# Performance work log

Measured on AMD Instinct MI355X. Metric: run time of the kernel, lower is better.

The kernel has to match this reference:

```python
import jax, jax.numpy as jnp
import numpy as np

T, B, NHID = 64, 32, 768
NB, BS = 6, 128          # num_blocks, block_size = nhid // num_blocks
TOPK = 4                 # active blocks per step
NTOK = 32000
ATT = 4 * BS             # input-attention value dim (att_out), per RIMs BlocksCore
DK = 64                  # input-attention key dim
NH2, DK2 = 4, 16         # communication attention heads / head dim


def setup_inputs() -> dict:
    key = jax.random.key(0)
    ks = jax.random.split(key, 16)
    s = 0.02
    return {
        "x": jax.random.normal(ks[0], (T, B, NHID), jnp.float32),
        "hx0": jax.random.normal(ks[1], (B, NHID), jnp.float32),
        "cx0": jax.random.normal(ks[2], (B, NHID), jnp.float32),
        # input attention (1 head): per-read-block query proj, per-write-slot key/value proj
        "Wq_in": jax.random.normal(ks[3], (NB, BS, DK), jnp.float32) * s,
        "Wk_in": jax.random.normal(ks[4], (2, NHID, DK), jnp.float32) * s,
        "Wv_in": jax.random.normal(ks[5], (2, NHID, ATT), jnp.float32) * s,
        # block-diagonal LSTM (blockify_params): per-block weights
        "Wih": jax.random.normal(ks[6], (NB, ATT, 4 * BS), jnp.float32) * s,
        "Whh": jax.random.normal(ks[7], (NB, BS, 4 * BS), jnp.float32) * s,
        "b_lstm": jnp.zeros((NB, 4 * BS), jnp.float32),
        # communication attention (4 heads, dk=dv=16), per-block projections + output proj
        "Wq_c": jax.random.normal(ks[8], (NB, BS, NH2 * DK2), jnp.float32) * s,
        "Wk_c": jax.random.normal(ks[9], (NB, BS, NH2 * DK2), jnp.float32) * s,
        "Wv_c": jax.random.normal(ks[10], (NB, BS, NH2 * DK2), jnp.float32) * s,
        "Wo_c": jax.random.normal(ks[11], (NB, NH2 * DK2, BS), jnp.float32) * s,
        # decoder
        "Wd": jax.random.normal(ks[12], (NTOK, NHID), jnp.float32) * 0.1,
        "bd": jnp.zeros((NTOK,), jnp.float32),
    }


def _step(hx, cx, xt, Wq_in, Wk_in, Wv_in, Wih, Whh, b_lstm, Wq_c, Wk_c, Wv_c, Wo_c):
    hb = hx.reshape(B, NB, BS)
    cb = cx.reshape(B, NB, BS)
    # --- input attention: each block reads from {null, input} slots ---
    kv_in = jnp.stack([jnp.zeros_like(xt), xt], axis=1)          # [B,2,NHID]
    q = jnp.einsum('bnd,ndk->bnk', hb, Wq_in)                    # [B,NB,DK]
    k = jnp.einsum('bmd,mdk->bmk', kv_in, Wk_in)                 # [B,2,DK]
    v = jnp.einsum('bmd,mdv->bmv', kv_in, Wv_in)                 # [B,2,ATT]
    iatt = jax.nn.softmax(
        jnp.einsum('bnk,bmk->bnm', q, k) / jnp.sqrt(jnp.float32(DK)), axis=-1)
    inp_use = jnp.einsum('bnm,bmv->bnv', iatt, v)                # [B,NB,ATT]
    # --- top-k block routing: drop NB-TOPK blocks attending most to null ---
    null_att = iatt[:, :, 0]                                     # [B,NB]
    _, drop_idx = jax.lax.top_k(null_att, NB - TOPK)
    mask = jnp.ones((B, NB), hx.dtype).at[
        jnp.arange(B)[:, None], drop_idx].set(0.0)               # [B,NB]
    # --- per-block (block-diagonal) LSTM ---
    gates = (jnp.einsum('bnv,nvg->bng', inp_use, Wih)
             + jnp.einsum('bnh,nhg->bng', hb, Whh) + b_lstm)     # [B,NB,4*BS]
    i, f, g, o = jnp.split(gates, 4, axis=-1)
    c_new = jax.nn.sigmoid(f) * cb + jax.nn.sigmoid(i) * jnp.tanh(g)
    h_new = jax.nn.sigmoid(o) * jnp.tanh(c_new)                  # [B,NB,BS]
    # --- communication attention among blocks (residual) ---
    q2 = jnp.einsum('bnd,ndk->bnk', h_new, Wq_c).reshape(B, NB, NH2, DK2)
    k2 = jnp.einsum('bnd,ndk->bnk', h_new, Wk_c).reshape(B, NB, NH2, DK2)
    v2 = jnp.einsum('bnd,ndk->bnk', h_new, Wv_c).reshape(B, NB, NH2, DK2)
    att = jax.nn.softmax(
        jnp.einsum('bihk,bjhk->bhij', q2, k2) / jnp.sqrt(jnp.float32(DK2)), axis=-1)
    comm = jnp.einsum('bhij,bjhv->bihv', att, v2).reshape(B, NB, NH2 * DK2)
    h_new = h_new + jnp.einsum('bnk,nkd->bnd', comm, Wo_c)
    # --- gated state update: inactive blocks keep old state ---
    m = mask[:, :, None]
    hx_next = (m * h_new + (1.0 - m) * hb).reshape(B, NHID)
    cx_next = (m * c_new + (1.0 - m) * cb).reshape(B, NHID)
    return hx_next, cx_next


def reference(x, hx0, cx0, Wq_in, Wk_in, Wv_in, Wih, Whh, b_lstm,
              Wq_c, Wk_c, Wv_c, Wo_c, Wd, bd):
    def scan_step(carry, xt):
        hx, cx = carry
        hx, cx = _step(hx, cx, xt, Wq_in, Wk_in, Wv_in, Wih, Whh, b_lstm,
                       Wq_c, Wk_c, Wv_c, Wo_c)
        return (hx, cx), hx
    (hx, cx), outs = jax.lax.scan(scan_step, (hx0, cx0), x)     # outs: [T,B,NHID]
    decoded = outs.reshape(T * B, NHID) @ Wd.T + bd              # [T*B,NTOK]
    return decoded, hx, cx
```

## Files before the change

kernel.cpp:

```cpp
#include <hip/hip_runtime.h>
#include <hip/hip_bf16.h>
#include <stdint.h>

#define TT 64
#define BB 32
#define NHIDC 768
#define NBK 6
#define BSZ 128
#define NTOKC 32000

using f32x4  = __attribute__((ext_vector_type(4))) float;
using f32x2  = __attribute__((ext_vector_type(2))) float;
using short8 = __attribute__((ext_vector_type(8))) short;
typedef unsigned long long u64;

#define OFF_XPUB  4096u
#define OFF_WTH   1048576u
#define OFF_WTL   4194304u
#define OFF_HTB   8065024u
#define OFF_K1    11210752u
#define OFF_V1H   11735040u
#define OFF_V1L   13832192u
#define OFF_U     15929344u
#define OFF_WDB   41095168u

__device__ __forceinline__ float sigf(float x){ return 1.f/(1.f + expf(-x)); }

__device__ __forceinline__ void stp(u64* p, float v, unsigned tag){
  union { float f; unsigned u; } cv; cv.f = v;
  const u64 pk = ((u64)tag << 32) | cv.u;
  __hip_atomic_store(p, pk, __ATOMIC_RELAXED, __HIP_MEMORY_SCOPE_AGENT);
}
__device__ __forceinline__ float ldp(const u64* p, unsigned tag){
  u64 v = __hip_atomic_load(p, __ATOMIC_RELAXED, __HIP_MEMORY_SCOPE_AGENT);
  while ((unsigned)(v >> 32) < tag){
    __builtin_amdgcn_s_sleep(1);
    v = __hip_atomic_load(p, __ATOMIC_RELAXED, __HIP_MEMORY_SCOPE_AGENT);
  }
  union { unsigned u; float f; } cv; cv.u = (unsigned)v;
  return cv.f;
}
#define CBAR asm volatile("" ::: "memory")

__device__ __forceinline__ void gload16(const void* g, void* l){
  __builtin_amdgcn_global_load_lds(
      (const __attribute__((address_space(1))) unsigned int*)g,
      (__attribute__((address_space(3))) unsigned int*)l, 16, 0, 0);
}

__device__ __forceinline__ int xslot(int par, int gg, int nn, int b){
  return (((par*16 + gg)*6 + nn)*2 + b)*132;
}

__device__ __forceinline__ void split_hl(float v, unsigned short& h16, unsigned short& l16){
  __hip_bfloat16 h = __float2bfloat16(v);
  float hv = __bfloat162float(h);
  __hip_bfloat16 l = __float2bfloat16(v - hv);
  h16 = *reinterpret_cast<unsigned short*>(&h);
  l16 = *reinterpret_cast<unsigned short*>(&l);
}

template<int TM, int TN>
__device__ void gemm_tile(const float* __restrict__ A, int lda,
                          const float* __restrict__ Bb, int ldb,
                          float* __restrict__ Cb, int ldc,
                          int N, int K, int m0, int n0,
                          float* AsP, float* BsP, int tid)
{
  constexpr int BM = 16*TM, BN = 16*TN;
  float (*As)[BM]   = reinterpret_cast<float(*)[BM]>(AsP);
  float (*Bs)[BN+4] = reinterpret_cast<float(*)[BN+4]>(BsP);
  const int tx = tid & 15, ty = tid >> 4;
  float acc[TM][TN];
  #pragma unroll
  for (int i=0;i<TM;++i)
    #pragma unroll
    for (int j=0;j<TN;++j) acc[i][j]=0.f;

  for (int k0=0; k0<K; k0+=16){
    {
      const int r = tid>>2, kk = (tid&3)*4;
      const float4 v0 = *(const float4*)&A[(long)(m0+r)*lda + k0 + kk];
      As[kk+0][r]=v0.x; As[kk+1][r]=v0.y; As[kk+2][r]=v0.z; As[kk+3][r]=v0.w;
    }
    {
      const int rb = tid>>4, cb = (tid&15)*4;
      float4 v0 = {0,0,0,0};
      if (n0+cb+4 <= N) v0 = *(const float4*)&Bb[(long)(k0+rb)*ldb + n0+cb];
      *(float4*)&Bs[rb][cb] = v0;
    }
    __syncthreads();
    #pragma unroll
    for (int kk=0; kk<16; ++kk){
      float av[TM], bv[TN];
      #pragma unroll
      for (int i=0;i<TM;++i) av[i] = As[kk][ty*TM+i];
      #pragma unroll
      for (int j=0;j<TN;++j) bv[j] = Bs[kk][tx*TN+j];
      #pragma unroll
      for (int i=0;i<TM;++i)
        #pragma unroll
        for (int j=0;j<TN;++j) acc[i][j] += av[i]*bv[j];
    }
    __syncthreads();
  }
  #pragma unroll
  for (int i=0;i<TM;++i){
    const int row = m0 + ty*TM + i;
    #pragma unroll
    for (int j=0;j<TN;++j){
      const int col = n0 + tx*TN + j;
      if (col < N) Cb[(long)row*ldc + col] = acc[i][j];
    }
  }
}

__device__ void gemm_tile_v1(const float* __restrict__ A,
                             const float* __restrict__ Bb,
                             unsigned short* __restrict__ V1H,
                             unsigned short* __restrict__ V1L,
                             int m0, int n0,
                             float* AsP, float* BsP, int tid)
{
  float (*As)[64] = reinterpret_cast<float(*)[64]>(AsP);
  float (*Bs)[68] = reinterpret_cast<float(*)[68]>(BsP);
  const int tx = tid & 15, ty = tid >> 4;
  float acc[4][4];
  #pragma unroll
  for (int i=0;i<4;++i)
    #pragma unroll
    for (int j=0;j<4;++j) acc[i][j]=0.f;

  for (int k0=0; k0<768; k0+=16){
    {
      const int r = tid>>2, kk = (tid&3)*4;
      const float4 v0 = *(const float4*)&A[(long)(m0+r)*768 + k0 + kk];
      As[kk+0][r]=v0.x; As[kk+1][r]=v0.y; As[kk+2][r]=v0.z; As[kk+3][r]=v0.w;
    }
    {
      const int rb = tid>>4, cb = (tid&15)*4;
      const float4 v0 = *(const float4*)&Bb[(long)(k0+rb)*512 + n0+cb];
      *(float4*)&Bs[rb][cb] = v0;
    }
    __syncthreads();
    #pragma unroll
    for (int kk=0; kk<16; ++kk){
      float av[4], bv[4];
      #pragma unroll
      for (int i=0;i<4;++i) av[i] = As[kk][ty*4+i];
      #pragma unroll
      for (int j=0;j<4;++j) bv[j] = Bs[kk][tx*4+j];
      #pragma unroll
      for (int i=0;i<4;++i)
        #pragma unroll
        for (int j=0;j<4;++j) acc[i][j] += av[i]*bv[j];
    }
    __syncthreads();
  }
  #pragma unroll
  for (int i=0;i<4;++i){
    const int row = m0 + ty*4 + i;
    const int col0 = n0 + tx*4;
    ushort4 oh, ol;
    split_hl(acc[i][0], oh.x, ol.x);
    split_hl(acc[i][1], oh.y, ol.y);
    split_hl(acc[i][2], oh.z, ol.z);
    split_hl(acc[i][3], oh.w, ol.w);
    *(ushort4*)&V1H[(long)row*512 + col0] = oh;
    *(ushort4*)&V1L[(long)row*512 + col0] = ol;
  }
}

__global__ __launch_bounds__(256) void pre1_kernel(
    const float* __restrict__ x,
    const float* __restrict__ Wk_in, const float* __restrict__ Wv_in,
    const float* __restrict__ Wih,
    float* __restrict__ K1b,
    unsigned short* __restrict__ V1H, unsigned short* __restrict__ V1L,
    unsigned short* __restrict__ WTH, unsigned short* __restrict__ WTL,
    u64* __restrict__ xpub)
{
  __shared__ float As[16*64];
  __shared__ float Bs[16*68];
  __shared__ float T[64][65];
  const int bid = blockIdx.x, tid = threadIdx.x;
  if (bid < 32){
    gemm_tile<4,4>(x, 768, Wk_in + 768*64, 64, K1b, 64, 64, 768,
                   bid*64, 0, As, Bs, tid);
  } else if (bid < 288){
    const int v = bid - 32;
    gemm_tile_v1(x, Wv_in + 768*512, V1H, V1L,
                 (v>>3)*64, (v&7)*64, As, Bs, tid);
  } else if (bid < 352){
    const int nx = 2*16*6*2*132;
    for (int i = (bid-288)*256 + tid; i < nx; i += 64*256)
      __hip_atomic_store(&xpub[i], 0ull, __ATOMIC_RELAXED, __HIP_MEMORY_SCOPE_AGENT);
  } else {
    const int tb = bid - 352;
    const int z = tb>>6, tile = tb&63, kt = (tile>>3)<<6, ct = (tile&7)<<6;
    const float* src = Wih + (long)z*262144;
    #pragma unroll 4
    for (int i=0;i<16;++i){
      const int idx = i*256+tid, rr = idx>>6, cc = idx&63;
      T[rr][cc] = src[(long)(kt+rr)*512 + ct+cc];
    }
    __syncthreads();
    #pragma unroll 4
    for (int i=0;i<16;++i){
      const int idx = i*256+tid, cr = idx>>6, kk = idx&63;
      unsigned short h16, l16;
      split_hl(T[kk][cr], h16, l16);
      WTH[(long)z*262144 + (long)(ct+cr)*512 + kt+kk] = h16;
      WTL[(long)z*262144 + (long)(ct+cr)*512 + kt+kk] = l16;
    }
  }
}

__global__ __launch_bounds__(256) void pre2_kernel(
    const unsigned short* __restrict__ V1H, const unsigned short* __restrict__ V1L,
    const unsigned short* __restrict__ WTH, const unsigned short* __restrict__ WTL,
    const float* __restrict__ Wd,
    float* __restrict__ Ub, unsigned short* __restrict__ Wdb)
{
  __shared__ unsigned short AH[4096], AL[4096], BH[4096], BL[4096];
  const int bid = blockIdx.x, tid = threadIdx.x;
  if (bid < 384){
    const int z = bid%6, mt = (bid/6)%16, nt2 = bid/96;
    const int m0 = mt*128, n0 = nt2*128;
    const int wv = tid>>6, lane = tid&63;
    const int wm = wv>>1, wn = wv&1;
    const int r16 = lane&15, krow = lane>>4;
    f32x4 acc[4][4] = {};
    const unsigned short* Bh = WTH + (long)z*262144;
    const unsigned short* Bl = WTL + (long)z*262144;

    for (int k0 = 0; k0 < 512; k0 += 32){
      #pragma unroll
      for (int i=0; i<2; ++i){
        const int idx = i*256 + tid;
        const int row = idx >> 2, k8 = (idx & 3)*8;
        gload16(&V1H[(long)(m0+row)*512 + k0 + k8], (char*)AH + i*4096 + wv*1024);
        gload16(&V1L[(long)(m0+row)*512 + k0 + k8], (char*)AL + i*4096 + wv*1024);
        gload16(&Bh [(long)(n0+row)*512 + k0 + k8], (char*)BH + i*4096 + wv*1024);
        gload16(&Bl [(long)(n0+row)*512 + k0 + k8], (char*)BL + i*4096 + wv*1024);
      }
      __syncthreads();
      short8 ah[4], al[4], bh[4], bl[4];
      #pragma unroll
      for (int mi=0; mi<4; ++mi){
        const int off = (wm*64 + mi*16 + r16)*32 + krow*8;
        ah[mi] = *(const short8*)&AH[off];
        al[mi] = *(const short8*)&AL[off];
      }
      #pragma unroll
      for (int ni=0; ni<4; ++ni){
        const int off = (wn*64 + ni*16 + r16)*32 + krow*8;
        bh[ni] = *(const short8*)&BH[off];
        bl[ni] = *(const short8*)&BL[off];
      }
      #pragma unroll
      for (int mi=0; mi<4; ++mi)
        #pragma unroll
        for (int ni=0; ni<4; ++ni){
          acc[mi][ni] = __builtin_amdgcn_mfma_f32_16x16x32_bf16(ah[mi], bh[ni], acc[mi][ni], 0, 0, 0);
          acc[mi][ni] = __builtin_amdgcn_mfma_f32_16x16x32_bf16(ah[mi], bl[ni], acc[mi][ni], 0, 0, 0);
          acc[mi][ni] = __builtin_amdgcn_mfma_f32_16x16x32_bf16(al[mi], bh[ni], acc[mi][ni], 0, 0, 0);
        }
      __syncthreads();
    }
    #pragma unroll
    for (int ni=0; ni<4; ++ni){
      const int col = n0 + wn*64 + ni*16 + r16;
      #pragma unroll
      for (int mi=0; mi<4; ++mi){
        const int rbase = m0 + wm*64 + mi*16 + krow*4;
        #pragma unroll
        for (int j=0; j<4; ++j)
          Ub[(long)(rbase + j)*3072 + z*512 + col] = acc[mi][ni][j];
      }
    }
  } else {
    const long n4 = (long)NTOKC*NHIDC/4;
    for (long i = (long)(bid-384)*256 + tid; i < n4; i += (long)384*256){
      const float4 v = ((const float4*)Wd)[i];
      ushort4 o;
      __hip_bfloat16 b0 = __float2bfloat16(v.x); o.x = *reinterpret_cast<unsigned short*>(&b0);
      __hip_bfloat16 b1 = __float2bfloat16(v.y); o.y = *reinterpret_cast<unsigned short*>(&b1);
      __hip_bfloat16 b2 = __float2bfloat16(v.z); o.z = *reinterpret_cast<unsigned short*>(&b2);
      __hip_bfloat16 b3 = __float2bfloat16(v.w); o.w = *reinterpret_cast<unsigned short*>(&b3);
      ((ushort4*)Wdb)[i] = o;
    }
  }
}

__global__ __launch_bounds__(1024, 2) void recurrent_kernel(
    const float* __restrict__ hx0, const float* __restrict__ cx0,
    const float* __restrict__ Wq_in, const float* __restrict__ Whh,
    const float* __restrict__ b_lstm,
    const float* __restrict__ Wk_c, const float* __restrict__ Wv_c,
    const float* __restrict__ Wq_c, const float* __restrict__ Wo_c,
    const float* __restrict__ K1buf, const float* __restrict__ Ubuf,
    u64* __restrict__ xpub,
    unsigned short* __restrict__ HTx,
    float* __restrict__ out_hx, float* __restrict__ out_cx)
{
  const int w = blockIdx.x, gg = w/6, n = w - gg*6, tid = threadIdx.x;

  __shared__ float WcT[192*130];
  __shared__ float WqL[128*65];
  __shared__ float hL[2][128], cL[2][128], h0L[2][128], cnL[2][128];
  __shared__ float partL[2][2][512];
  __shared__ float uL[2][512];
  __shared__ float blL[512];
  __shared__ float kvqL[2][192];
  __shared__ float kvAll[2][6][130];
  __shared__ float commL[2][64];
  __shared__ float nullAll[2][8];
  __shared__ float sL[2], nullLoc[2], maskL[2];

  const int kh = tid >> 9, gc = tid & 511;
  const int od = tid >> 3, okq = tid & 7;

  f32x4 whr[16];
  {
    const float* src = Whh + (long)n*65536 + kh*64*512 + gc;
    #pragma unroll
    for (int r4=0; r4<16; ++r4){
      f32x4 v;
      v[0] = src[(r4*4+0)*512]; v[1] = src[(r4*4+1)*512];
      v[2] = src[(r4*4+2)*512]; v[3] = src[(r4*4+3)*512];
      whr[r4] = v;
    }
  }
  #pragma unroll
  for (int i=0;i<16;++i) asm volatile("" : "+v"(whr[i]));
  f32x4 wo0, wo1;
  {
    const float* src = Wo_c + n*8192 + od;
    #pragma unroll
    for (int j=0;j<4;++j) wo0[j] = src[(okq*8+j)*128];
    #pragma unroll
    for (int j=0;j<4;++j) wo1[j] = src[(okq*8+4+j)*128];
  }
  asm volatile("" : "+v"(wo0));
  asm volatile("" : "+v"(wo1));

  if (tid < 512) blL[tid] = b_lstm[n*512 + tid];
  for (int i = tid; i < 8192; i += 1024){
    const int h = i>>6, c = i&63;
    WcT[(c    )*130 + h] = Wk_c[n*8192 + i];
    WcT[(c+ 64)*130 + h] = Wv_c[n*8192 + i];
    WcT[(c+128)*130 + h] = Wq_c[n*8192 + i];
    WqL[h*65 + c] = Wq_in[n*8192 + i];
  }
  if (tid < 256){
    const int b = tid>>7, d = tid&127;
    hL[b][d] = hx0[(gg*2+b)*768 + n*128 + d];
    cL[b][d] = cx0[(gg*2+b)*768 + n*128 + d];
  }
  __syncthreads();

  for (int t = 0; t < TT; ++t){
    const int par = t & 1;
    const unsigned tag = (unsigned)(t+1);
    uL[kh][gc] = Ubuf[((long)(t*32 + gg*2 + kh)*6 + n)*512 + gc];
    float k1r = 0.f;
    if (tid < 128) k1r = K1buf[(long)(t*32 + gg*2 + (tid>>6))*64 + (tid&63)];

    {
      float gd0 = 0.f, gd1 = 0.f;
      #pragma unroll
      for (int r4 = 0; r4 < 16; ++r4){
        const f32x4 h0v = *(const f32x4*)&hL[0][kh*64 + r4*4];
        const f32x4 h1v = *(const f32x4*)&hL[1][kh*64 + r4*4];
        #pragma unroll
        for (int j=0;j<4;++j){
          gd0 += whr[r4][j]*h0v[j];
          gd1 += whr[r4][j]*h1v[j];
        }
      }
      partL[0][kh][gc] = gd0;
      partL[1][kh][gc] = gd1;
    }
    if (tid < 128){
      const int b = tid>>6, k = tid&63;
      float q = 0.f;
      #pragma unroll 16
      for (int h=0; h<128; ++h) q += WqL[h*65 + k]*hL[b][h];
      float term = q*k1r;
      #pragma unroll
      for (int off=32; off; off>>=1) term += __shfl_xor(term, off);
      if (k == 0){
        const float l1 = term*0.125f;
        const float mx = fmaxf(l1, 0.f);
        const float e0 = expf(0.f-mx), e1 = expf(l1-mx);
        const float inv = 1.f/(e0+e1);
        sL[b] = e1*inv;
        nullLoc[b] = e0*inv;
        stp(xpub + xslot(par,gg,n,b) + 128, e0*inv, tag);
      }
    }
    __syncthreads();
    if (tid < 256){
      const int b = tid>>7, dd = tid&127;
      const float s = sL[b];
      const float gi = partL[b][0][dd]     + partL[b][1][dd]     + s*uL[b][dd]     + blL[dd];
      const float gf = partL[b][0][128+dd] + partL[b][1][128+dd] + s*uL[b][128+dd] + blL[128+dd];
      const float gG = partL[b][0][256+dd] + partL[b][1][256+dd] + s*uL[b][256+dd] + blL[256+dd];
      const float go = partL[b][0][384+dd] + partL[b][1][384+dd] + s*uL[b][384+dd] + blL[384+dd];
      const float cp = cL[b][dd];
      const float cn = sigf(gf)*cp + sigf(gi)*tanhf(gG);
      const float h0 = sigf(go)*tanhf(cn);
      cnL[b][dd] = cn; h0L[b][dd] = h0;
    }
    __syncthreads();
    if (tid < 384){
      const int b = tid/192, c = tid%192;
      float a = 0.f;
      #pragma unroll
      for (int h4=0; h4<32; ++h4){
        const f32x2 wa = *(const f32x2*)&WcT[c*130 + h4*4];
        const f32x2 wb = *(const f32x2*)&WcT[c*130 + h4*4 + 2];
        const f32x4 hv = *(const f32x4*)&h0L[b][h4*4];
        a += wa[0]*hv[0] + wa[1]*hv[1] + wb[0]*hv[2] + wb[1]*hv[3];
      }
      kvqL[b][c] = a;
      if (c < 128) stp(xpub + xslot(par,gg,n,b) + c, a, tag);
    }
    __syncthreads();
    for (int idx = tid; idx < 1536; idx += 1024){
      const int j = idx/256, r = idx&255, b = r>>7, c = r&127;
      if (j == n) kvAll[b][j][c] = kvqL[b][c];
      else        kvAll[b][j][c] = ldp(xpub + xslot(par,gg,j,b) + c, tag);
    }
    if (tid < 12){
      const int j = tid>>1, b = tid&1;
      if (j == n) nullAll[b][j] = nullLoc[b];
      else        nullAll[b][j] = ldp(xpub + xslot(par,gg,j,b) + 128, tag);
    }
    __syncthreads(); CBAR;
    if (tid < 64){
      const int lane = tid;
      const int g5 = lane>>3, l3 = lane&7;
      const int b = g5>>2, h = g5&3;
      float lg = -1e30f;
      if (l3 < 6){
        float s = 0.f;
        #pragma unroll
        for (int kk=0; kk<16; ++kk)
          s += kvqL[b][128 + h*16 + kk]*kvAll[b][l3][h*16 + kk];
        lg = s*0.25f;
      }
      float mx = lg;
      mx = fmaxf(mx, __shfl_xor(mx,1));
      mx = fmaxf(mx, __shfl_xor(mx,2));
      mx = fmaxf(mx, __shfl_xor(mx,4));
      float ev = (l3 < 6) ? expf(lg - mx) : 0.f;
      float sum = ev;
      sum += __shfl_xor(sum,1); sum += __shfl_xor(sum,2); sum += __shfl_xor(sum,4);
      const float myw = ev/sum;
      float s0 = 0.f, s1 = 0.f;
      #pragma unroll
      for (int j=0;j<6;++j){
        const float wj = __shfl(myw, g5*8 + j);
        s0 += wj*kvAll[b][j][64 + h*16 + l3*2];
        s1 += wj*kvAll[b][j][64 + h*16 + l3*2 + 1];
      }
      commL[b][h*16 + l3*2]     = s0;
      commL[b][h*16 + l3*2 + 1] = s1;
      if (lane < 2){
        const float own = nullAll[lane][n];
        int rank = 0;
        #pragma unroll
        for (int j=0;j<6;++j){
          const float v = nullAll[lane][j];
          rank += (v > own || (v == own && j < n)) ? 1 : 0;
        }
        maskL[lane] = (rank < 2) ? 0.f : 1.f;
      }
    }
    __syncthreads();
    {
      #pragma unroll
      for (int b=0; b<2; ++b){
        float a = 0.f;
        #pragma unroll
        for (int j=0;j<4;++j) a += commL[b][okq*8+j]*wo0[j];
        #pragma unroll
        for (int j=0;j<4;++j) a += commL[b][okq*8+4+j]*wo1[j];
        a += __shfl_xor(a,1); a += __shfl_xor(a,2); a += __shfl_xor(a,4);
        if (okq == 0 && maskL[b] != 0.f){
          hL[b][od] = h0L[b][od] + a;
          cL[b][od] = cnL[b][od];
        }
      }
    }
    __syncthreads();
    if (tid < 256){
      const int b = tid>>7, d = tid&127;
      const float hv = hL[b][d];
      __hip_bfloat16 hb16 = __float2bfloat16(hv);
      HTx[(long)(t*32 + gg*2 + b)*768 + n*128 + d] = *reinterpret_cast<unsigned short*>(&hb16);
      if (t == TT-1){
        out_hx[(gg*2+b)*768 + n*128 + d] = hv;
        out_cx[(gg*2+b)*768 + n*128 + d] = cL[b][d];
      }
    }
  }
}

__global__ __launch_bounds__(256) void decoder_kernel(
    const unsigned short* __restrict__ A,
    const unsigned short* __restrict__ Bw,
    const float* __restrict__ bd,
    float* __restrict__ out)
{
  __shared__ unsigned short As[8192];
  __shared__ unsigned short Bs[8192];
  const int bid = blockIdx.x;
  const int tile = (bid & 7)*500 + (bid >> 3);
  const int m0 = (tile & 15)*128, n0 = (tile >> 4)*128;
  const int tid = threadIdx.x;
  const int wv = tid >> 6, lane = tid & 63;
  const int wm = wv >> 1, wn = wv & 1;
  const int r16 = lane & 15, krow = lane >> 4;

  f32x4 acc[4][4] = {};

  for (int k0 = 0; k0 < 768; k0 += 64){
    #pragma unroll
    for (int i=0; i<4; ++i){
      const int idx = i*256 + tid;
      const int row = idx >> 3, cp = idx & 7;
      const int csrc = cp ^ (row & 7);
      gload16(&A [(long)(m0+row)*768 + k0 + csrc*8], (char*)As + i*4096 + wv*1024);
      gload16(&Bw[(long)(n0+row)*768 + k0 + csrc*8], (char*)Bs + i*4096 + wv*1024);
    }
    __syncthreads();
    short8 af[4][2], bf[4][2];
    #pragma unroll
    for (int mi=0; mi<4; ++mi){
      const int row = wm*64 + mi*16 + r16;
      #pragma unroll
      for (int ks=0; ks<2; ++ks){
        const int kc = ks*4 + krow;
        af[mi][ks] = *(const short8*)&As[row*64 + ((kc ^ (row&7))<<3)];
      }
    }
    #pragma unroll
    for (int ni=0; ni<4; ++ni){
      const int row = wn*64 + ni*16 + r16;
      #pragma unroll
      for (int ks=0; ks<2; ++ks){
        const int kc = ks*4 + krow;
        bf[ni][ks] = *(const short8*)&Bs[row*64 + ((kc ^ (row&7))<<3)];
      }
    }
    #pragma unroll
    for (int mi=0; mi<4; ++mi)
      #pragma unroll
      for (int ni=0; ni<4; ++ni){
        acc[mi][ni] = __builtin_amdgcn_mfma_f32_16x16x32_bf16(af[mi][0], bf[ni][0], acc[mi][ni], 0, 0, 0);
        acc[mi][ni] = __builtin_amdgcn_mfma_f32_16x16x32_bf16(af[mi][1], bf[ni][1], acc[mi][ni], 0, 0, 0);
      }
    __syncthreads();
  }

  #pragma unroll
  for (int ni=0; ni<4; ++ni){
    const int col = n0 + wn*64 + ni*16 + r16;
    const float bv = bd[col];
    #pragma unroll
    for (int mi=0; mi<4; ++mi){
      const int rbase = m0 + wm*64 + mi*16 + krow*4;
      #pragma unroll
      for (int j=0; j<4; ++j)
        out[(size_t)(rbase + j)*NTOKC + col] = acc[mi][ni][j] + bv;
    }
  }
}

extern "C" void kernel_launch(void* const* d_in, const int* in_sizes, int n_in,
                              void* d_out, int out_size, void* d_ws, size_t ws_size,
                              hipStream_t stream)
{
  (void)in_sizes; (void)n_in; (void)out_size; (void)ws_size;
  const float* x      = (const float*)d_in[0];
  const float* hx0    = (const float*)d_in[1];
  const float* cx0    = (const float*)d_in[2];
  const float* Wq_in  = (const float*)d_in[3];
  const float* Wk_in  = (const float*)d_in[4];
  const float* Wv_in  = (const float*)d_in[5];
  const float* Wih    = (const float*)d_in[6];
  const float* Whh    = (const float*)d_in[7];
  const float* b_lstm = (const float*)d_in[8];
  const float* Wq_c   = (const float*)d_in[9];
  const float* Wk_c   = (const float*)d_in[10];
  const float* Wv_c   = (const float*)d_in[11];
  const float* Wo_c   = (const float*)d_in[12];
  const float* Wd     = (const float*)d_in[13];
  const float* bd     = (const float*)d_in[14];

  char* ws = (char*)d_ws;
  u64*           xpub = (u64*)(ws + OFF_XPUB);
  unsigned short* WTH = (unsigned short*)(ws + OFF_WTH);
  unsigned short* WTL = (unsigned short*)(ws + OFF_WTL);
  unsigned short* HTx = (unsigned short*)(ws + OFF_HTB);
  float*         K1b  = (float*)(ws + OFF_K1);
  unsigned short* V1H = (unsigned short*)(ws + OFF_V1H);
  unsigned short* V1L = (unsigned short*)(ws + OFF_V1L);
  float*         Ub   = (float*)(ws + OFF_U);
  unsigned short* Wdb = (unsigned short*)(ws + OFF_WDB);

  float* out_dec = (float*)d_out;
  float* out_hx  = out_dec + (size_t)2048*NTOKC;
  float* out_cx  = out_hx + BB*NHIDC;

  pre1_kernel<<<736, 256, 0, stream>>>(x, Wk_in, Wv_in, Wih, K1b,
                                       V1H, V1L, WTH, WTL, xpub);
  pre2_kernel<<<768, 256, 0, stream>>>(V1H, V1L, WTH, WTL, Wd, Ub, Wdb);
  recurrent_kernel<<<96, 1024, 0, stream>>>(hx0, cx0, Wq_in, Whh, b_lstm,
                                            Wk_c, Wv_c, Wq_c, Wo_c,
                                            K1b, Ub, xpub, HTx,
                                            out_hx, out_cx);
  decoder_kernel<<<4000, 256, 0, stream>>>(HTx, Wdb, bd, out_dec);
}
```

Before: 1.127 ms.

## Add L2-scoped fast-path flag exchange with fallback to agent-scope atomics

```diff
diff --git a/kernel.cpp b/kernel.cpp
--- a/kernel.cpp
+++ b/kernel.cpp
@@ -17,6 +17,7 @@
 #define OFF_XPUB  4096u
 #define OFF_WTH   1048576u
 #define OFF_WTL   4194304u
+#define OFF_FPUB  7340032u
 #define OFF_HTB   8065024u
 #define OFF_K1    11210752u
 #define OFF_V1H   11735040u
@@ -39,6 +40,19 @@
   }
   union { unsigned u; float f; } cv; cv.u = (unsigned)v;
   return cv.f;
+}
+__device__ __forceinline__ void st8_l2(u64* p, u64 v){
+  asm volatile("global_store_dwordx2 %0, %1, off sc0" :: "v"(p), "v"(v) : "memory");
+}
+__device__ __forceinline__ u64 ld8_l2(const u64* p){
+  u64 r;
+  asm volatile("global_load_dwordx2 %0, %1, off sc0\n\ts_waitcnt vmcnt(0)"
+               : "=v"(r) : "v"(p) : "memory");
+  return r;
+}
+__device__ __forceinline__ u64 packtv(float v, unsigned tag){
+  union { float f; unsigned u; } cv; cv.f = v;
+  return ((u64)tag << 32) | cv.u;
 }
 #define CBAR asm volatile("" ::: "memory")
 
@@ -178,7 +192,7 @@
     float* __restrict__ K1b,
     unsigned short* __restrict__ V1H, unsigned short* __restrict__ V1L,
     unsigned short* __restrict__ WTH, unsigned short* __restrict__ WTL,
-    u64* __restrict__ xpub)
+    u64* __restrict__ xpub, u64* __restrict__ fpub)
 {
   __shared__ float As[16*64];
   __shared__ float Bs[16*68];
@@ -193,8 +207,10 @@
                  (v>>3)*64, (v&7)*64, As, Bs, tid);
   } else if (bid < 352){
     const int nx = 2*16*6*2*132;
-    for (int i = (bid-288)*256 + tid; i < nx; i += 64*256)
-      __hip_atomic_store(&xpub[i], 0ull, __ATOMIC_RELAXED, __HIP_MEMORY_SCOPE_AGENT);
+    for (int i = (bid-288)*256 + tid; i < nx; i += 64*256){
+      xpub[i] = 0ull;
+      fpub[i] = 0ull;
+    }
   } else {
     const int tb = bid - 352;
     const int z = tb>>6, tile = tb&63, kt = (tile>>3)<<6, ct = (tile&7)<<6;
@@ -300,11 +316,11 @@
     const float* __restrict__ Wk_c, const float* __restrict__ Wv_c,
     const float* __restrict__ Wq_c, const float* __restrict__ Wo_c,
     const float* __restrict__ K1buf, const float* __restrict__ Ubuf,
-    u64* __restrict__ xpub,
+    u64* __restrict__ xpub, u64* __restrict__ fpub,
     unsigned short* __restrict__ HTx,
     float* __restrict__ out_hx, float* __restrict__ out_cx)
 {
-  const int w = blockIdx.x, gg = w/6, n = w - gg*6, tid = threadIdx.x;
+  const int w = blockIdx.x, gg = w & 15, n = w >> 4, tid = threadIdx.x;
 
   __shared__ float WcT[192*130];
   __shared__ float WqL[128*65];
@@ -360,6 +376,8 @@
   }
   __syncthreads();
 
+  bool fastOK = true;
+
   for (int t = 0; t < TT; ++t){
     const int par = t & 1;
     const unsigned tag = (unsigned)(t+1);
@@ -397,6 +415,7 @@
         const float inv = 1.f/(e0+e1);
         sL[b] = e1*inv;
         nullLoc[b] = e0*inv;
+        st8_l2(fpub + xslot(par,gg,n,b) + 128, packtv(e0*inv, tag));
         stp(xpub + xslot(par,gg,n,b) + 128, e0*inv, tag);
       }
     }
@@ -425,18 +444,59 @@
         a += wa[0]*hv[0] + wa[1]*hv[1] + wb[0]*hv[2] + wb[1]*hv[3];
       }
       kvqL[b][c] = a;
-      if (c < 128) stp(xpub + xslot(par,gg,n,b) + c, a, tag);
+      if (c < 128){
+        st8_l2(fpub + xslot(par,gg,n,b) + c, packtv(a, tag));
+        stp(xpub + xslot(par,gg,n,b) + c, a, tag);
+      }
     }
     __syncthreads();
     for (int idx = tid; idx < 1536; idx += 1024){
       const int j = idx/256, r = idx&255, b = r>>7, c = r&127;
-      if (j == n) kvAll[b][j][c] = kvqL[b][c];
-      else        kvAll[b][j][c] = ldp(xpub + xslot(par,gg,j,b) + c, tag);
+      float val;
+      if (j == n){
+        val = kvqL[b][c];
+      } else {
+        const int slot = xslot(par,gg,j,b) + c;
+        bool got = false; val = 0.f;
+        if (fastOK){
+          int tries = 0;
+          for(;;){
+            const u64 v = ld8_l2(fpub + slot);
+            if ((unsigned)(v >> 32) >= tag){
+              union { unsigned u; float f; } cv; cv.u = (unsigned)v;
+              val = cv.f; got = true; break;
+            }
+            if (++tries > 64){ fastOK = false; break; }
+            __builtin_amdgcn_s_sleep(1);
+          }
+        }
+        if (!got) val = ldp(xpub + slot, tag);
+      }
+      kvAll[b][j][c] = val;
     }
     if (tid < 12){
       const int j = tid>>1, b = tid&1;
-      if (j == n) nullAll[b][j] = nullLoc[b];
-      else        nullAll[b][j] = ldp(xpub + xslot(par,gg,j,b) + 128, tag);
+      float val;
+      if (j == n){
+        val = nullLoc[b];
+      } else {
+        const int slot = xslot(par,gg,j,b) + 128;
+        bool got = false; val = 0.f;
+        if (fastOK){
+          int tries = 0;
+          for(;;){
+            const u64 v = ld8_l2(fpub + slot);
+            if ((unsigned)(v >> 32) >= tag){
+              union { unsigned u; float f; } cv; cv.u = (unsigned)v;
+              val = cv.f; got = true; break;
+            }
+            if (++tries > 64){ fastOK = false; break; }
+            __builtin_amdgcn_s_sleep(1);
+          }
+        }
+        if (!got) val = ldp(xpub + slot, tag);
+      }
+      nullAll[b][j] = val;
     }
     __syncthreads(); CBAR;
     if (tid < 64){
@@ -603,6 +663,7 @@
 
   char* ws = (char*)d_ws;
   u64*           xpub = (u64*)(ws + OFF_XPUB);
+  u64*           fpub = (u64*)(ws + OFF_FPUB);
   unsigned short* WTH = (unsigned short*)(ws + OFF_WTH);
   unsigned short* WTL = (unsigned short*)(ws + OFF_WTL);
   unsigned short* HTx = (unsigned short*)(ws + OFF_HTB);
@@ -617,11 +678,11 @@
   float* out_cx  = out_hx + BB*NHIDC;
 
   pre1_kernel<<<736, 256, 0, stream>>>(x, Wk_in, Wv_in, Wih, K1b,
-                                       V1H, V1L, WTH, WTL, xpub);
+                                       V1H, V1L, WTH, WTL, xpub, fpub);
   pre2_kernel<<<768, 256, 0, stream>>>(V1H, V1L, WTH, WTL, Wd, Ub, Wdb);
   recurrent_kernel<<<96, 1024, 0, stream>>>(hx0, cx0, Wq_in, Whh, b_lstm,
                                             Wk_c, Wv_c, Wq_c, Wo_c,
-                                            K1b, Ub, xpub, HTx,
+                                            K1b, Ub, xpub, fpub, HTx,
                                             out_hx, out_cx);
   decoder_kernel<<<4000, 256, 0, stream>>>(HTx, Wdb, bd, out_dec);
 }
```

After: 1.185 ms. +5.1%, slower.

## Process two batch-pair groups per recurrent block, halving grid to 48 blocks

Applied to the files above, without the earlier changes.

```diff
diff --git a/kernel.cpp b/kernel.cpp
--- a/kernel.cpp
+++ b/kernel.cpp
@@ -293,7 +293,7 @@
   }
 }
 
-__global__ __launch_bounds__(1024, 2) void recurrent_kernel(
+__global__ __launch_bounds__(1024, 1) void recurrent_kernel(
     const float* __restrict__ hx0, const float* __restrict__ cx0,
     const float* __restrict__ Wq_in, const float* __restrict__ Whh,
     const float* __restrict__ b_lstm,
@@ -304,19 +304,20 @@
     unsigned short* __restrict__ HTx,
     float* __restrict__ out_hx, float* __restrict__ out_cx)
 {
-  const int w = blockIdx.x, gg = w/6, n = w - gg*6, tid = threadIdx.x;
+  const int w = blockIdx.x, n = w % 6, pairI = w / 6, tid = threadIdx.x;
+  const int g0 = pairI*2, g1 = pairI*2 + 1;
 
   __shared__ float WcT[192*130];
   __shared__ float WqL[128*65];
-  __shared__ float hL[2][128], cL[2][128], h0L[2][128], cnL[2][128];
+  __shared__ float blL[512];
   __shared__ float partL[2][2][512];
-  __shared__ float uL[2][512];
-  __shared__ float blL[512];
-  __shared__ float kvqL[2][192];
+  __shared__ float hL[2][2][128], cL[2][2][128];
+  __shared__ float h0L[2][2][128], cnL[2][2][128];
+  __shared__ float kvqL[2][2][192];
   __shared__ float kvAll[2][6][130];
   __shared__ float commL[2][64];
   __shared__ float nullAll[2][8];
-  __shared__ float sL[2], nullLoc[2], maskL[2];
+  __shared__ float sL[2][2], nullLoc[2][2], maskL[2][2];
 
   const int kh = tid >> 9, gc = tid & 511;
   const int od = tid >> 3, okq = tid & 7;
@@ -353,158 +354,184 @@
     WcT[(c+128)*130 + h] = Wq_c[n*8192 + i];
     WqL[h*65 + c] = Wq_in[n*8192 + i];
   }
-  if (tid < 256){
-    const int b = tid>>7, d = tid&127;
-    hL[b][d] = hx0[(gg*2+b)*768 + n*128 + d];
-    cL[b][d] = cx0[(gg*2+b)*768 + n*128 + d];
+  if (tid < 512){
+    const int gi = tid >> 8, r = tid & 255;
+    const int b = r >> 7, d = r & 127;
+    const int gth = (gi ? g1 : g0);
+    hL[gi][b][d] = hx0[(gth*2+b)*768 + n*128 + d];
+    cL[gi][b][d] = cx0[(gth*2+b)*768 + n*128 + d];
   }
   __syncthreads();
 
   for (int t = 0; t < TT; ++t){
     const int par = t & 1;
     const unsigned tag = (unsigned)(t+1);
-    uL[kh][gc] = Ubuf[((long)(t*32 + gg*2 + kh)*6 + n)*512 + gc];
-    float k1r = 0.f;
-    if (tid < 128) k1r = K1buf[(long)(t*32 + gg*2 + (tid>>6))*64 + (tid&63)];
-
-    {
-      float gd0 = 0.f, gd1 = 0.f;
-      #pragma unroll
-      for (int r4 = 0; r4 < 16; ++r4){
-        const f32x4 h0v = *(const f32x4*)&hL[0][kh*64 + r4*4];
-        const f32x4 h1v = *(const f32x4*)&hL[1][kh*64 + r4*4];
-        #pragma unroll
-        for (int j=0;j<4;++j){
-          gd0 += whr[r4][j]*h0v[j];
-          gd1 += whr[r4][j]*h1v[j];
-        }
-      }
-      partL[0][kh][gc] = gd0;
-      partL[1][kh][gc] = gd1;
-    }
-    if (tid < 128){
-      const int b = tid>>6, k = tid&63;
-      float q = 0.f;
-      #pragma unroll 16
-      for (int h=0; h<128; ++h) q += WqL[h*65 + k]*hL[b][h];
-      float term = q*k1r;
-      #pragma unroll
-      for (int off=32; off; off>>=1) term += __shfl_xor(term, off);
-      if (k == 0){
-        const float l1 = term*0.125f;
-        const float mx = fmaxf(l1, 0.f);
-        const float e0 = expf(0.f-mx), e1 = expf(l1-mx);
-        const float inv = 1.f/(e0+e1);
-        sL[b] = e1*inv;
-        nullLoc[b] = e0*inv;
-        stp(xpub + xslot(par,gg,n,b) + 128, e0*inv, tag);
-      }
-    }
-    __syncthreads();
+
+    float u0[2], u1[2], u2[2], u3[2], k1r[2];
     if (tid < 256){
       const int b = tid>>7, dd = tid&127;
-      const float s = sL[b];
-      const float gi = partL[b][0][dd]     + partL[b][1][dd]     + s*uL[b][dd]     + blL[dd];
-      const float gf = partL[b][0][128+dd] + partL[b][1][128+dd] + s*uL[b][128+dd] + blL[128+dd];
-      const float gG = partL[b][0][256+dd] + partL[b][1][256+dd] + s*uL[b][256+dd] + blL[256+dd];
-      const float go = partL[b][0][384+dd] + partL[b][1][384+dd] + s*uL[b][384+dd] + blL[384+dd];
-      const float cp = cL[b][dd];
-      const float cn = sigf(gf)*cp + sigf(gi)*tanhf(gG);
-      const float h0 = sigf(go)*tanhf(cn);
-      cnL[b][dd] = cn; h0L[b][dd] = h0;
-    }
-    __syncthreads();
-    if (tid < 384){
-      const int b = tid/192, c = tid%192;
-      float a = 0.f;
-      #pragma unroll
-      for (int h4=0; h4<32; ++h4){
-        const f32x2 wa = *(const f32x2*)&WcT[c*130 + h4*4];
-        const f32x2 wb = *(const f32x2*)&WcT[c*130 + h4*4 + 2];
-        const f32x4 hv = *(const f32x4*)&h0L[b][h4*4];
-        a += wa[0]*hv[0] + wa[1]*hv[1] + wb[0]*hv[2] + wb[1]*hv[3];
-      }
-      kvqL[b][c] = a;
-      if (c < 128) stp(xpub + xslot(par,gg,n,b) + c, a, tag);
-    }
-    __syncthreads();
-    for (int idx = tid; idx < 1536; idx += 1024){
-      const int j = idx/256, r = idx&255, b = r>>7, c = r&127;
-      if (j == n) kvAll[b][j][c] = kvqL[b][c];
-      else        kvAll[b][j][c] = ldp(xpub + xslot(par,gg,j,b) + c, tag);
-    }
-    if (tid < 12){
-      const int j = tid>>1, b = tid&1;
-      if (j == n) nullAll[b][j] = nullLoc[b];
-      else        nullAll[b][j] = ldp(xpub + xslot(par,gg,j,b) + 128, tag);
-    }
-    __syncthreads(); CBAR;
-    if (tid < 64){
-      const int lane = tid;
-      const int g5 = lane>>3, l3 = lane&7;
-      const int b = g5>>2, h = g5&3;
-      float lg = -1e30f;
-      if (l3 < 6){
-        float s = 0.f;
-        #pragma unroll
-        for (int kk=0; kk<16; ++kk)
-          s += kvqL[b][128 + h*16 + kk]*kvAll[b][l3][h*16 + kk];
-        lg = s*0.25f;
-      }
-      float mx = lg;
-      mx = fmaxf(mx, __shfl_xor(mx,1));
-      mx = fmaxf(mx, __shfl_xor(mx,2));
-      mx = fmaxf(mx, __shfl_xor(mx,4));
-      float ev = (l3 < 6) ? expf(lg - mx) : 0.f;
-      float sum = ev;
-      sum += __shfl_xor(sum,1); sum += __shfl_xor(sum,2); sum += __shfl_xor(sum,4);
-      const float myw = ev/sum;
-      float s0 = 0.f, s1 = 0.f;
-      #pragma unroll
-      for (int j=0;j<6;++j){
-        const float wj = __shfl(myw, g5*8 + j);
-        s0 += wj*kvAll[b][j][64 + h*16 + l3*2];
-        s1 += wj*kvAll[b][j][64 + h*16 + l3*2 + 1];
-      }
-      commL[b][h*16 + l3*2]     = s0;
-      commL[b][h*16 + l3*2 + 1] = s1;
-      if (lane < 2){
-        const float own = nullAll[lane][n];
-        int rank = 0;
+      #pragma unroll
+      for (int gi=0; gi<2; ++gi){
+        const int gth = (gi ? g1 : g0);
+        const long ub = ((long)(t*32 + gth*2 + b)*6 + n)*512 + dd;
+        u0[gi]=Ubuf[ub]; u1[gi]=Ubuf[ub+128]; u2[gi]=Ubuf[ub+256]; u3[gi]=Ubuf[ub+384];
+      }
+    }
+    if (tid < 128){
+      #pragma unroll
+      for (int gi=0; gi<2; ++gi){
+        const int gth = (gi ? g1 : g0);
+        k1r[gi] = K1buf[(long)(t*32 + gth*2 + (tid>>6))*64 + (tid&63)];
+      }
+    }
+
+    #pragma unroll
+    for (int gi=0; gi<2; ++gi){
+      const int gth = (gi ? g1 : g0);
+      {
+        float gd0 = 0.f, gd1 = 0.f;
+        #pragma unroll
+        for (int r4 = 0; r4 < 16; ++r4){
+          const f32x4 h0v = *(const f32x4*)&hL[gi][0][kh*64 + r4*4];
+          const f32x4 h1v = *(const f32x4*)&hL[gi][1][kh*64 + r4*4];
+          #pragma unroll
+          for (int j=0;j<4;++j){
+            gd0 += whr[r4][j]*h0v[j];
+            gd1 += whr[r4][j]*h1v[j];
+          }
+        }
+        partL[0][kh][gc] = gd0;
+        partL[1][kh][gc] = gd1;
+      }
+      if (tid < 128){
+        const int b = tid>>6, k = tid&63;
+        float q = 0.f;
+        #pragma unroll 16
+        for (int h=0; h<128; ++h) q += WqL[h*65 + k]*hL[gi][b][h];
+        float term = q*k1r[gi];
+        #pragma unroll
+        for (int off=32; off; off>>=1) term += __shfl_xor(term, off);
+        if (k == 0){
+          const float l1 = term*0.125f;
+          const float mx = fmaxf(l1, 0.f);
+          const float e0 = expf(0.f-mx), e1 = expf(l1-mx);
+          const float inv = 1.f/(e0+e1);
+          sL[gi][b] = e1*inv;
+          nullLoc[gi][b] = e0*inv;
+          stp(xpub + xslot(par,gth,n,b) + 128, e0*inv, tag);
+        }
+      }
+      __syncthreads();
+      if (tid < 256){
+        const int b = tid>>7, dd = tid&127;
+        const float s = sL[gi][b];
+        const float gI = partL[b][0][dd]     + partL[b][1][dd]     + s*u0[gi] + blL[dd];
+        const float gF = partL[b][0][128+dd] + partL[b][1][128+dd] + s*u1[gi] + blL[128+dd];
+        const float gG = partL[b][0][256+dd] + partL[b][1][256+dd] + s*u2[gi] + blL[256+dd];
+        const float gO = partL[b][0][384+dd] + partL[b][1][384+dd] + s*u3[gi] + blL[384+dd];
+        const float cp = cL[gi][b][dd];
+        const float cn = sigf(gF)*cp + sigf(gI)*tanhf(gG);
+        const float h0 = sigf(gO)*tanhf(cn);
+        cnL[gi][b][dd] = cn; h0L[gi][b][dd] = h0;
+      }
+      __syncthreads();
+      if (tid < 384){
+        const int b = tid/192, c = tid%192;
+        float a = 0.f;
+        #pragma unroll
+        for (int h4=0; h4<32; ++h4){
+          const f32x2 wa = *(const f32x2*)&WcT[c*130 + h4*4];
+          const f32x2 wb = *(const f32x2*)&WcT[c*130 + h4*4 + 2];
+          const f32x4 hv = *(const f32x4*)&h0L[gi][b][h4*4];
+          a += wa[0]*hv[0] + wa[1]*hv[1] + wb[0]*hv[2] + wb[1]*hv[3];
+        }
+        kvqL[gi][b][c] = a;
+        if (c < 128) stp(xpub + xslot(par,gth,n,b) + c, a, tag);
+      }
+      __syncthreads();
+    }
+
+    #pragma unroll
+    for (int gi=0; gi<2; ++gi){
+      const int gth = (gi ? g1 : g0);
+      for (int idx = tid; idx < 1536; idx += 1024){
+        const int j = idx/256, r = idx&255, b = r>>7, c = r&127;
+        if (j == n) kvAll[b][j][c] = kvqL[gi][b][c];
+        else        kvAll[b][j][c] = ldp(xpub + xslot(par,gth,j,b) + c, tag);
+      }
+      if (tid < 12){
+        const int j = tid>>1, b = tid&1;
+        if (j == n) nullAll[b][j] = nullLoc[gi][b];
+        else        nullAll[b][j] = ldp(xpub + xslot(par,gth,j,b) + 128, tag);
+      }
+      __syncthreads(); CBAR;
+      if (tid < 64){
+        const int lane = tid;
+        const int g5 = lane>>3, l3 = lane&7;
+        const int b = g5>>2, h = g5&3;
+        float lg = -1e30f;
+        if (l3 < 6){
+          float s = 0.f;
+          #pragma unroll
+          for (int kk=0; kk<16; ++kk)
+            s += kvqL[gi][b][128 + h*16 + kk]*kvAll[b][l3][h*16 + kk];
+          lg = s*0.25f;
+        }
+        float mx = lg;
+        mx = fmaxf(mx, __shfl_xor(mx,1));
+        mx = fmaxf(mx, __shfl_xor(mx,2));
+        mx = fmaxf(mx, __shfl_xor(mx,4));
+        float ev = (l3 < 6) ? expf(lg - mx) : 0.f;
+        float sum = ev;
+        sum += __shfl_xor(sum,1); sum += __shfl_xor(sum,2); sum += __shfl_xor(sum,4);
+        const float myw = ev/sum;
+        float s0 = 0.f, s1 = 0.f;
         #pragma unroll
         for (int j=0;j<6;++j){
-          const float v = nullAll[lane][j];
-          rank += (v > own || (v == own && j < n)) ? 1 : 0;
-        }
-        maskL[lane] = (rank < 2) ? 0.f : 1.f;
-      }
-    }
-    __syncthreads();
-    {
-      #pragma unroll
-      for (int b=0; b<2; ++b){
-        float a = 0.f;
-        #pragma unroll
-        for (int j=0;j<4;++j) a += commL[b][okq*8+j]*wo0[j];
-        #pragma unroll
-        for (int j=0;j<4;++j) a += commL[b][okq*8+4+j]*wo1[j];
-        a += __shfl_xor(a,1); a += __shfl_xor(a,2); a += __shfl_xor(a,4);
-        if (okq == 0 && maskL[b] != 0.f){
-          hL[b][od] = h0L[b][od] + a;
-          cL[b][od] = cnL[b][od];
-        }
-      }
-    }
-    __syncthreads();
-    if (tid < 256){
-      const int b = tid>>7, d = tid&127;
-      const float hv = hL[b][d];
-      __hip_bfloat16 hb16 = __float2bfloat16(hv);
-      HTx[(long)(t*32 + gg*2 + b)*768 + n*128 + d] = *reinterpret_cast<unsigned short*>(&hb16);
-      if (t == TT-1){
-        out_hx[(gg*2+b)*768 + n*128 + d] = hv;
-        out_cx[(gg*2+b)*768 + n*128 + d] = cL[b][d];
-      }
+          const float wj = __shfl(myw, g5*8 + j);
+          s0 += wj*kvAll[b][j][64 + h*16 + l3*2];
+          s1 += wj*kvAll[b][j][64 + h*16 + l3*2 + 1];
+        }
+        commL[b][h*16 + l3*2]     = s0;
+        commL[b][h*16 + l3*2 + 1] = s1;
+        if (lane < 2){
+          const float own = nullAll[lane][n];
+          int rank = 0;
+          #pragma unroll
+          for (int j=0;j<6;++j){
+            const float v = nullAll[lane][j];
+            rank += (v > own || (v == own && j < n)) ? 1 : 0;
+          }
+          maskL[gi][lane] = (rank < 2) ? 0.f : 1.f;
+        }
+      }
+      __syncthreads();
+      {
+        #pragma unroll
+        for (int b=0; b<2; ++b){
+          float a = 0.f;
+          #pragma unroll
+          for (int j=0;j<4;++j) a += commL[b][okq*8+j]*wo0[j];
+          #pragma unroll
+          for (int j=0;j<4;++j) a += commL[b][okq*8+4+j]*wo1[j];
+          a += __shfl_xor(a,1); a += __shfl_xor(a,2); a += __shfl_xor(a,4);
+          if (okq == 0){
+            const bool mk = (maskL[gi][b] != 0.f);
+            const float hNew = mk ? (h0L[gi][b][od] + a) : hL[gi][b][od];
+            const float cNew = mk ? cnL[gi][b][od]       : cL[gi][b][od];
+            hL[gi][b][od] = hNew;
+            cL[gi][b][od] = cNew;
+            __hip_bfloat16 hb16 = __float2bfloat16(hNew);
+            HTx[(long)(t*32 + gth*2 + b)*768 + n*128 + od] =
+                *reinterpret_cast<unsigned short*>(&hb16);
+            if (t == TT-1){
+              out_hx[(gth*2+b)*768 + n*128 + od] = hNew;
+              out_cx[(gth*2+b)*768 + n*128 + od] = cNew;
+            }
+          }
+        }
+      }
+      __syncthreads();
     }
   }
 }
@@ -619,7 +646,7 @@
   pre1_kernel<<<736, 256, 0, stream>>>(x, Wk_in, Wv_in, Wih, K1b,
                                        V1H, V1L, WTH, WTL, xpub);
   pre2_kernel<<<768, 256, 0, stream>>>(V1H, V1L, WTH, WTL, Wd, Ub, Wdb);
-  recurrent_kernel<<<96, 1024, 0, stream>>>(hx0, cx0, Wq_in, Whh, b_lstm,
+  recurrent_kernel<<<48, 1024, 0, stream>>>(hx0, cx0, Wq_in, Whh, b_lstm,
                                             Wk_c, Wv_c, Wq_c, Wo_c,
                                             K1b, Ub, xpub, HTx,
                                             out_hx, out_cx);
```

After: 1.910 ms. 1.69x slower.
